# Optimization experiments

Hardware: AMD Instinct MI355X
Metric: run time of the kernel (lower is better)

The kernel has to match this reference:

```python
import jax, jax.numpy as jnp
import numpy as np

EPS = 1e-7


def ciou_pairwise(b1, b2):
    # b1: (N,1,4), b2: (1,N,4) in xyxy; returns (N,N) CIoU
    b1x1, b1y1, b1x2, b1y2 = b1[..., 0], b1[..., 1], b1[..., 2], b1[..., 3]
    b2x1, b2y1, b2x2, b2y2 = b2[..., 0], b2[..., 1], b2[..., 2], b2[..., 3]

    # intersection
    iw = jnp.clip(jnp.minimum(b1x2, b2x2) - jnp.maximum(b1x1, b2x1), 0.0)
    ih = jnp.clip(jnp.minimum(b1y2, b2y2) - jnp.maximum(b1y1, b2y1), 0.0)
    inter = iw * ih

    w1, h1 = b1x2 - b1x1, b1y2 - b1y1
    w2, h2 = b2x2 - b2x1, b2y2 - b2y1
    union = w1 * h1 + w2 * h2 - inter + EPS
    iou = inter / union

    # smallest enclosing box diagonal
    cw = jnp.maximum(b1x2, b2x2) - jnp.minimum(b1x1, b2x1)
    ch = jnp.maximum(b1y2, b2y2) - jnp.minimum(b1y1, b2y1)
    c2 = cw * cw + ch * ch + EPS

    # squared center distance
    rho2 = ((b2x1 + b2x2 - b1x1 - b1x2) ** 2 + (b2y1 + b2y2 - b1y1 - b1y2) ** 2) / 4.0

    # aspect-ratio consistency term
    v = (4.0 / (np.pi ** 2)) * (jnp.arctan(w2 / (h2 + EPS)) - jnp.arctan(w1 / (h1 + EPS))) ** 2
    alpha = jax.lax.stop_gradient(v / (v - iou + (1.0 + EPS)))
    return iou - (rho2 / c2 + v * alpha)


def setup_inputs() -> dict:
    key = jax.random.key(0)
    k1, k2, k3 = jax.random.split(key, 3)
    N = 4096
    conf = jax.random.uniform(k1, (N, 1), dtype=jnp.float32)           # confidence in [0,1)
    xy1 = jax.random.uniform(k2, (N, 2), dtype=jnp.float32) * 600.0    # top-left corner
    wh = jax.random.uniform(k3, (N, 2), dtype=jnp.float32) * 100.0 + 1.0  # width/height >= 1
    x = jnp.concatenate([conf, xy1, xy1 + wh], axis=1)                 # (N, 5): conf, x1, y1, x2, y2
    gamma = jnp.zeros((1,), dtype=jnp.float32)
    return {"x": x, "gamma": gamma}


def reference(x, gamma):
    boxes = x[:, 1:]
    conf = x[:, 0]
    iou = ciou_pairwise(boxes[:, None, :], boxes[None, :, :])          # (N, N)
    conf_matrix = conf[:, None] * conf[None, :]                        # (N, N) outer product
    attention = jax.nn.softmax(iou * conf_matrix, axis=-1)             # (N, N)
    x_prime = x * gamma + attention @ x                                # (N, 5)
    return jax.nn.sigmoid(x_prime)
```

## Files before the change

### kernel.cpp

```cpp
#include <hip/hip_runtime.h>
#include <math.h>

#define N 4096
#define FEPS 1e-7f
#define ROWS 4
#define BLK 256

__global__ __launch_bounds__(BLK) void ciou_attn_kernel(
        const float* __restrict__ x,
        const float* __restrict__ gamma,
        float* __restrict__ out) {
    const int tid = threadIdx.x;
    const int i0 = blockIdx.x * ROWS;

    float rx1[ROWS], ry1[ROWS], rx2[ROWS], ry2[ROWS];
    float rsx[ROWS], rsy[ROWS], rar[ROWS], rat[ROWS], rcf[ROWS];
#pragma unroll
    for (int r = 0; r < ROWS; r++) {
        const float* xi = x + (size_t)(i0 + r) * 5;
        float cf = xi[0], x1 = xi[1], y1 = xi[2], x2 = xi[3], y2 = xi[4];
        float w = x2 - x1, h = y2 - y1;
        rcf[r] = cf;
        rx1[r] = x1; ry1[r] = y1; rx2[r] = x2; ry2[r] = y2;
        rsx[r] = x1 + x2; rsy[r] = y1 + y2;
        rar[r] = w * h;
        rat[r] = atanf(w / (h + FEPS));
    }

    float sum[ROWS];
    float acc[ROWS][5];
#pragma unroll
    for (int r = 0; r < ROWS; r++) {
        sum[r] = 0.f;
#pragma unroll
        for (int c = 0; c < 5; c++) acc[r][c] = 0.f;
    }

    const float K = 0.4052847345693511f;

    for (int j = tid; j < N; j += BLK) {
        const float* xj = x + (size_t)j * 5;
        float jcf = xj[0], jx1 = xj[1], jy1 = xj[2], jx2 = xj[3], jy2 = xj[4];
        float jw = jx2 - jx1, jh = jy2 - jy1;
        float jsx = jx1 + jx2, jsy = jy1 + jy2;
        float jar = jw * jh;
        float jat = atanf(jw / (jh + FEPS));
#pragma unroll
        for (int r = 0; r < ROWS; r++) {
            float iw = fminf(rx2[r], jx2) - fmaxf(rx1[r], jx1);
            iw = fmaxf(iw, 0.f);
            float ih = fminf(ry2[r], jy2) - fmaxf(ry1[r], jy1);
            ih = fmaxf(ih, 0.f);
            float inter = iw * ih;
            float uni = rar[r] + jar - inter + FEPS;
            float iou = inter * __builtin_amdgcn_rcpf(uni);
            iou = fminf(iou, 1.0f);
            float cw = fmaxf(rx2[r], jx2) - fminf(rx1[r], jx1);
            float ch = fmaxf(ry2[r], jy2) - fminf(ry1[r], jy1);
            float c2 = cw * cw + ch * ch + FEPS;
            float dx = jsx - rsx[r];
            float dy = jsy - rsy[r];
            float rho2 = (dx * dx + dy * dy) * 0.25f;
            float da = jat - rat[r];
            float v = K * da * da;
            float alpha = v * __builtin_amdgcn_rcpf(v - iou + (1.f + FEPS));
            float ciou = iou - (rho2 * __builtin_amdgcn_rcpf(c2) + v * alpha);
            float s = ciou * rcf[r] * jcf;
            float e = __expf(s);
            sum[r] += e;
            acc[r][0] += e * jcf;
            acc[r][1] += e * jx1;
            acc[r][2] += e * jy1;
            acc[r][3] += e * jx2;
            acc[r][4] += e * jy2;
        }
    }

    __shared__ float red[BLK / 64][ROWS * 6];
    const int wave = tid >> 6;
    const int lane = tid & 63;
#pragma unroll
    for (int r = 0; r < ROWS; r++) {
        float v6[6] = {sum[r], acc[r][0], acc[r][1], acc[r][2], acc[r][3], acc[r][4]};
#pragma unroll
        for (int k = 0; k < 6; k++) {
            float val = v6[k];
#pragma unroll
            for (int off = 32; off > 0; off >>= 1) val += __shfl_down(val, off, 64);
            if (lane == 0) red[wave][r * 6 + k] = val;
        }
    }
    __syncthreads();
    if (tid < ROWS * 6) {
        float tot = 0.f;
#pragma unroll
        for (int w = 0; w < BLK / 64; w++) tot += red[w][tid];
        red[0][tid] = tot;
    }
    __syncthreads();
    if (tid < ROWS * 5) {
        int r = tid / 5, c = tid % 5;
        int i = i0 + r;
        float se = red[0][r * 6];
        float a = red[0][r * 6 + 1 + c];
        float xp = x[(size_t)i * 5 + c] * gamma[0] + a / se;
        out[(size_t)i * 5 + c] = 1.f / (1.f + expf(-xp));
    }
}

extern "C" void kernel_launch(void* const* d_in, const int* in_sizes, int n_in,
                              void* d_out, int out_size, void* d_ws, size_t ws_size,
                              hipStream_t stream) {
    const float* x = (const float*)d_in[0];
    const float* gamma = (const float*)d_in[1];
    float* out = (float*)d_out;
    ciou_attn_kernel<<<N / ROWS, BLK, 0, stream>>>(x, gamma, out);
}
```

Baseline: 92.75 us.

## Precompute per-box features in a prepass and simplify the CIoU inner loop

```diff
diff --git a/kernel.cpp b/kernel.cpp
--- a/kernel.cpp
+++ b/kernel.cpp
@@ -3,28 +3,40 @@
 
 #define N 4096
 #define FEPS 1e-7f
-#define ROWS 4
+#define ROWS 8
 #define BLK 256
+#define FSTRIDE 12
+
+__global__ void precompute_kernel(const float* __restrict__ x, float* __restrict__ f) {
+    int i = blockIdx.x * blockDim.x + threadIdx.x;
+    if (i >= N) return;
+    float cf = x[i * 5 + 0], x1 = x[i * 5 + 1], y1 = x[i * 5 + 2];
+    float x2 = x[i * 5 + 3], y2 = x[i * 5 + 4];
+    float w = x2 - x1, h = y2 - y1;
+    float* fi = f + (size_t)i * FSTRIDE;
+    fi[0] = cf; fi[1] = x1; fi[2] = y1; fi[3] = x2; fi[4] = y2;
+    fi[5] = x1 + x2; fi[6] = y1 + y2; fi[7] = w; fi[8] = h;
+    fi[9] = w * h + FEPS;
+    fi[10] = atanf(w / (h + FEPS));
+    fi[11] = w * h;
+}
 
 __global__ __launch_bounds__(BLK) void ciou_attn_kernel(
         const float* __restrict__ x,
+        const float* __restrict__ f,
         const float* __restrict__ gamma,
         float* __restrict__ out) {
     const int tid = threadIdx.x;
     const int i0 = blockIdx.x * ROWS;
 
-    float rx1[ROWS], ry1[ROWS], rx2[ROWS], ry2[ROWS];
-    float rsx[ROWS], rsy[ROWS], rar[ROWS], rat[ROWS], rcf[ROWS];
+    float rx1[ROWS], ry1[ROWS], rx2[ROWS], ry2[ROWS], rsx[ROWS], rsy[ROWS];
+    float rw[ROWS], rh[ROWS], rar[ROWS], rat[ROWS], rcf[ROWS];
 #pragma unroll
     for (int r = 0; r < ROWS; r++) {
-        const float* xi = x + (size_t)(i0 + r) * 5;
-        float cf = xi[0], x1 = xi[1], y1 = xi[2], x2 = xi[3], y2 = xi[4];
-        float w = x2 - x1, h = y2 - y1;
-        rcf[r] = cf;
-        rx1[r] = x1; ry1[r] = y1; rx2[r] = x2; ry2[r] = y2;
-        rsx[r] = x1 + x2; rsy[r] = y1 + y2;
-        rar[r] = w * h;
-        rat[r] = atanf(w / (h + FEPS));
+        const float* fi = f + (size_t)(i0 + r) * FSTRIDE;
+        rcf[r] = fi[0]; rx1[r] = fi[1]; ry1[r] = fi[2]; rx2[r] = fi[3]; ry2[r] = fi[4];
+        rsx[r] = fi[5]; rsy[r] = fi[6]; rw[r] = fi[7]; rh[r] = fi[8];
+        rar[r] = fi[11]; rat[r] = fi[10];
     }
 
     float sum[ROWS];
@@ -37,36 +49,36 @@
     }
 
     const float K = 0.4052847345693511f;
+    const float ONEP = 1.f + FEPS;
 
+#pragma unroll 2
     for (int j = tid; j < N; j += BLK) {
-        const float* xj = x + (size_t)j * 5;
-        float jcf = xj[0], jx1 = xj[1], jy1 = xj[2], jx2 = xj[3], jy2 = xj[4];
-        float jw = jx2 - jx1, jh = jy2 - jy1;
-        float jsx = jx1 + jx2, jsy = jy1 + jy2;
-        float jar = jw * jh;
-        float jat = atanf(jw / (jh + FEPS));
+        const float4* fj = (const float4*)(f + (size_t)j * FSTRIDE);
+        float4 A = fj[0], B = fj[1], C = fj[2];
+        float jcf = A.x, jx1 = A.y, jy1 = A.z, jx2 = A.w;
+        float jy2 = B.x, jsx = B.y, jsy = B.z, jw = B.w;
+        float jh = C.x, jar2 = C.y, jat = C.z;
 #pragma unroll
         for (int r = 0; r < ROWS; r++) {
-            float iw = fminf(rx2[r], jx2) - fmaxf(rx1[r], jx1);
-            iw = fmaxf(iw, 0.f);
-            float ih = fminf(ry2[r], jy2) - fmaxf(ry1[r], jy1);
-            ih = fmaxf(ih, 0.f);
+            float iwr = fminf(rx2[r], jx2) - fmaxf(rx1[r], jx1);
+            float ihr = fminf(ry2[r], jy2) - fmaxf(ry1[r], jy1);
+            float iw = fmaxf(iwr, 0.f);
+            float ih = fmaxf(ihr, 0.f);
             float inter = iw * ih;
-            float uni = rar[r] + jar - inter + FEPS;
-            float iou = inter * __builtin_amdgcn_rcpf(uni);
-            iou = fminf(iou, 1.0f);
-            float cw = fmaxf(rx2[r], jx2) - fminf(rx1[r], jx1);
-            float ch = fmaxf(ry2[r], jy2) - fminf(ry1[r], jy1);
+            float uni = (rar[r] + jar2) - inter;
+            float iou = fminf(inter * __builtin_amdgcn_rcpf(uni), 1.0f);
+            float cw = (rw[r] + jw) - iwr;
+            float ch = (rh[r] + jh) - ihr;
             float c2 = cw * cw + ch * ch + FEPS;
             float dx = jsx - rsx[r];
             float dy = jsy - rsy[r];
             float rho2 = (dx * dx + dy * dy) * 0.25f;
             float da = jat - rat[r];
             float v = K * da * da;
-            float alpha = v * __builtin_amdgcn_rcpf(v - iou + (1.f + FEPS));
-            float ciou = iou - (rho2 * __builtin_amdgcn_rcpf(c2) + v * alpha);
-            float s = ciou * rcf[r] * jcf;
-            float e = __expf(s);
+            float den = (v - iou) + ONEP;
+            float valpha = v * v * __builtin_amdgcn_rcpf(den);
+            float ciou = iou - (rho2 * __builtin_amdgcn_rcpf(c2) + valpha);
+            float e = __expf(ciou * rcf[r] * jcf);
             sum[r] += e;
             acc[r][0] += e * jcf;
             acc[r][1] += e * jx1;
@@ -114,5 +126,8 @@
     const float* x = (const float*)d_in[0];
     const float* gamma = (const float*)d_in[1];
     float* out = (float*)d_out;
-    ciou_attn_kernel<<<N / ROWS, BLK, 0, stream>>>(x, gamma, out);
+    float* f = (float*)d_ws;
+
+    precompute_kernel<<<(N + 255) / 256, 256, 0, stream>>>(x, f);
+    ciou_attn_kernel<<<N / ROWS, BLK, 0, stream>>>(x, f, gamma, out);
 }
```

Result: no change. 92.27 us (-0.5%).
